# Optimization experiments

Measured on AMD Instinct MI355X. Metric: run time of the kernel, lower is better.

The kernel has to match this reference:

```python
import jax, jax.numpy as jnp
import numpy as np

N = 50000      # nodes
E = 800000     # edges (avg degree 16)
IN = 128       # in_channels
OUT = 2        # out_channels
HID = 100 * OUT  # MAX_CHANNELS * out_channels = 200
MSG_EPS = 1e-7   # GENConv message eps
BN_EPS = 1e-5    # BatchNorm1d eps


def _gen_conv(x, src, dst, w1, b1, g, be, w2, b2):
    """PyG GENConv with defaults: aggr='softmax', t=1.0, msg_norm=False,
    MLP=[c, 2c, c_out] with BatchNorm1d+ReLU between layers (train-mode BN)."""
    # message: relu(x_j) + eps  -> [E, d]
    msg = jnp.maximum(x[src], 0.0) + MSG_EPS
    # scatter softmax over incoming edges of each destination node (t=1)
    m = jax.ops.segment_max(msg, dst, num_segments=N)          # [N, d]
    m = jnp.where(jnp.isfinite(m), m, 0.0)                      # isolated nodes
    ex = jnp.exp(msg - m[dst])                                  # [E, d]
    s = jax.ops.segment_sum(ex, dst, num_segments=N)            # [N, d]
    alpha = ex / (s[dst] + 1e-16)                               # [E, d]
    out = jax.ops.segment_sum(msg * alpha, dst, num_segments=N) # [N, d]
    out = out + x                                               # residual with x_dst
    # MLP: Linear -> BatchNorm(batch stats) -> ReLU -> Linear
    h = out @ w1 + b1                                           # [N, 2d]
    mu = h.mean(axis=0)
    var = h.var(axis=0)
    h = (h - mu) * jax.lax.rsqrt(var + BN_EPS) * g + be
    h = jnp.maximum(h, 0.0)
    return h @ w2 + b2


def setup_inputs() -> dict:
    key = jax.random.key(0)
    ks = jax.random.split(key, 8)
    rn = lambda k, shp, s: jax.random.normal(k, shp, jnp.float32) * s
    mid1, mid2 = 2 * IN, 2 * HID
    return {
        "x": rn(ks[0], (N, IN), 1.0),
        "edge_index": jax.random.randint(ks[1], (2, E), 0, N, jnp.int32),
        "c1_w1": rn(ks[2], (IN, mid1), 0.05), "c1_b1": jnp.zeros((mid1,), jnp.float32),
        "c1_g": jnp.ones((mid1,), jnp.float32), "c1_beta": jnp.zeros((mid1,), jnp.float32),
        "c1_w2": rn(ks[3], (mid1, HID), 0.05), "c1_b2": jnp.zeros((HID,), jnp.float32),
        "c2_w1": rn(ks[4], (HID, mid2), 0.05), "c2_b1": jnp.zeros((mid2,), jnp.float32),
        "c2_g": jnp.ones((mid2,), jnp.float32), "c2_beta": jnp.zeros((mid2,), jnp.float32),
        "c2_w2": rn(ks[5], (mid2, OUT), 0.05), "c2_b2": jnp.zeros((OUT,), jnp.float32),
    }


def reference(x, edge_index, c1_w1, c1_b1, c1_g, c1_beta, c1_w2, c1_b2,
              c2_w1, c2_b1, c2_g, c2_beta, c2_w2, c2_b2):
    src, dst = edge_index[0], edge_index[1]
    h = jnp.maximum(_gen_conv(x, src, dst, c1_w1, c1_b1, c1_g, c1_beta, c1_w2, c1_b2), 0.0)
    # Dropout(p=0.1) is identity in eval mode (deterministic reference)
    return jnp.maximum(_gen_conv(h, src, dst, c2_w1, c2_b1, c2_g, c2_beta, c2_w2, c2_b2), 0.0)
```

## Files before the change

### kernel.cpp

```cpp
#include <hip/hip_runtime.h>
#include <hip/hip_bf16.h>
#include <stdint.h>

#define NNODES 50000
#define NEDGES 800000
#define DIN 128
#define DHID 200
#define MID1 256
#define MID2 400
#define SCAN_NB ((NNODES + 255) / 256)
#define NBB ((NNODES + 127) / 128)
#define RSPLIT 12
#define LOG2E 1.4426950408889634f
#define LN2 0.6931471805599453f
#define GK_SPLIT 96
#define GCH 208
#define GNP 40
#define NBUCK 98
#define BCAP 16384
#define EPB 4096

typedef __hip_bfloat16 bf16;
typedef __attribute__((ext_vector_type(8))) short short8;
typedef __attribute__((ext_vector_type(4))) float floatx4;
typedef unsigned short ushort;

__device__ __forceinline__ float b2f(bf16 v) { return __bfloat162float(v); }
__device__ __forceinline__ bf16 f2b(float v) { return __float2bfloat16(v); }
__device__ __forceinline__ float bits2f(ushort b) {
    unsigned u = ((unsigned)b) << 16;
    return __uint_as_float(u);
}
__device__ __forceinline__ ushort f2bits(float f) {
    bf16 h = __float2bfloat16(f);
    return *(ushort*)&h;
}
__device__ __forceinline__ float ldin(const void* p, size_t i, int f32) {
    return f32 ? ((const float*)p)[i] : __bfloat162float(((const bf16*)p)[i]);
}
__device__ __forceinline__ void ldin4(const void* p, size_t i, int f32, float* v) {
    if (f32) {
        float4 f = *(const float4*)((const float*)p + i);
        v[0] = f.x; v[1] = f.y; v[2] = f.z; v[3] = f.w;
    } else {
        ushort4 u = *(const ushort4*)((const bf16*)p + i);
        v[0] = bits2f(u.x); v[1] = bits2f(u.y); v[2] = bits2f(u.z); v[3] = bits2f(u.w);
    }
}
__device__ __forceinline__ float fexp2(float x) {
#if __has_builtin(__builtin_amdgcn_exp2f)
    return __builtin_amdgcn_exp2f(x);
#else
    return exp2f(x);
#endif
}
__device__ __forceinline__ floatx4 mfma16(short8 a, short8 b, floatx4 c) {
    return __builtin_amdgcn_mfma_f32_16x16x32_bf16(a, b, c, 0, 0, 0);
}
__device__ __forceinline__ void acc4(ushort4 u, float* s, float* p) {
    ushort uu[4];
    *(ushort4*)uu = u;
#pragma unroll
    for (int c = 0; c < 4; c++) {
        float v = bits2f(uu[c]);
        float ee = fexp2(v);
        s[c] += ee;
        p[c] = fmaf(v, ee, p[c]);
    }
}

__global__ __launch_bounds__(256) void bin_kernel(const int* __restrict__ src,
                                                  const int* __restrict__ dst,
                                                  const void* __restrict__ g,
                                                  int* __restrict__ flag,
                                                  unsigned* __restrict__ bbuf,
                                                  int* __restrict__ gcur) {
    __shared__ int cnt[NBUCK], cur[NBUCK];
    int tid = threadIdx.x;
    if (blockIdx.x == 0 && tid == 0)
        *flag = (((const unsigned*)g)[0] == 0x3F800000u) ? 1 : 0;
    if (tid < NBUCK) cnt[tid] = 0;
    __syncthreads();
    int e0 = blockIdx.x * EPB;
    unsigned pk[16];
    int bk[16];
#pragma unroll
    for (int i = 0; i < 16; i++) {
        int e = e0 + i * 256 + tid;
        if (e < NEDGES) {
            int d = dst[e], s = src[e];
            pk[i] = ((unsigned)d << 16) | (unsigned)s;
            bk[i] = d >> 9;
            atomicAdd(&cnt[bk[i]], 1);
        } else {
            bk[i] = -1;
        }
    }
    __syncthreads();
    if (tid < NBUCK) cur[tid] = atomicAdd(&gcur[tid], cnt[tid]);
    __syncthreads();
#pragma unroll
    for (int i = 0; i < 16; i++) {
        if (bk[i] >= 0) {
            int off = atomicAdd(&cur[bk[i]], 1);
            bbuf[(size_t)bk[i] * BCAP + off] = pk[i];
        }
    }
}

__global__ __launch_bounds__(256) void histb_kernel(const unsigned* __restrict__ bbuf,
                                                    const int* __restrict__ gcur,
                                                    int* __restrict__ counts) {
    __shared__ int hc[512];
    int b = blockIdx.x, tid = threadIdx.x;
    int base = b << 9;
    int nn = min(512, NNODES - base);
    for (int i = tid; i < 512; i += 256) hc[i] = 0;
    __syncthreads();
    int cnt = gcur[b];
    const unsigned* eb = bbuf + (size_t)b * BCAP;
    for (int i = tid; i < cnt; i += 256) atomicAdd(&hc[(eb[i] >> 16) - base], 1);
    __syncthreads();
    for (int i = tid; i < nn; i += 256) counts[base + i] = hc[i];
}

__global__ __launch_bounds__(512) void scatterb_kernel(const unsigned* __restrict__ bbuf,
                                                       const int* __restrict__ gcur,
                                                       const int* __restrict__ rowptr,
                                                       int* __restrict__ ssrc) {
    __shared__ int lc[512];
    int b = blockIdx.x, tid = threadIdx.x;
    int base = b << 9;
    int nn = min(512, NNODES - base);
    lc[tid] = (tid < nn) ? rowptr[base + tid] : 0;
    __syncthreads();
    int cnt = gcur[b];
    const unsigned* eb = bbuf + (size_t)b * BCAP;
    for (int i = tid; i < cnt; i += 512) {
        unsigned p = eb[i];
        int node = (int)(p >> 16) - base;
        int idx = atomicAdd(&lc[node], 1);
        ssrc[idx] = (int)(p & 0xFFFFu);
    }
}

__global__ __launch_bounds__(256) void scanA_kernel(const int* __restrict__ counts,
                                                    int* __restrict__ rowptr,
                                                    int* __restrict__ blocksums) {
    __shared__ int sh[256];
    int t = threadIdx.x, b = blockIdx.x;
    int i = b * 256 + t;
    int v = (i < NNODES) ? counts[i] : 0;
    sh[t] = v;
    __syncthreads();
#pragma unroll
    for (int off = 1; off < 256; off <<= 1) {
        int o = (t >= off) ? sh[t - off] : 0;
        __syncthreads();
        sh[t] += o;
        __syncthreads();
    }
    if (i < NNODES) rowptr[i] = sh[t] - v;
    if (t == 255) blocksums[b] = sh[255];
}

__global__ __launch_bounds__(256) void scanC_kernel(int* __restrict__ rowptr,
                                                    const int* __restrict__ blocksums) {
    __shared__ int sh[256];
    int t = threadIdx.x, b = blockIdx.x;
    sh[t] = (t < SCAN_NB) ? blocksums[t] : 0;
    __syncthreads();
#pragma unroll
    for (int off = 1; off < 256; off <<= 1) {
        int o = (t >= off) ? sh[t - off] : 0;
        __syncthreads();
        sh[t] += o;
        __syncthreads();
    }
    int boff = (b > 0) ? sh[b - 1] : 0;
    int i = b * 256 + t;
    if (i < NNODES) rowptr[i] += boff;
    if (i == 0) rowptr[NNODES] = NEDGES;
}

#define TW (DIN * MID1 + MID1 * DHID + DHID * MID2)
__global__ __launch_bounds__(256) void prep_kernel(const void* __restrict__ W1, bf16* __restrict__ Wt1,
                                                   const void* __restrict__ W2, bf16* __restrict__ Wt2,
                                                   const void* __restrict__ W3, bf16* __restrict__ Wt3,
                                                   const void* __restrict__ X, bf16* __restrict__ M1,
                                                   ushort* __restrict__ dummy,
                                                   const int* __restrict__ flag) {
    const int S1 = DIN * MID1, S2 = MID1 * DHID;
    int f32 = *flag;
    int idx = blockIdx.x * 256 + threadIdx.x;
    if (idx < TW) {
        const void* W;
        bf16* Wt;
        int K, N, li;
        if (idx < S1) { W = W1; Wt = Wt1; K = DIN; N = MID1; li = idx; }
        else if (idx < S1 + S2) { W = W2; Wt = Wt2; K = MID1; N = DHID; li = idx - S1; }
        else { W = W3; Wt = Wt3; K = DHID; N = MID2; li = idx - S1 - S2; }
        int k = li / N, n = li - k * N;
        Wt[(size_t)n * K + k] = f2b(ldin(W, li, f32));
    }
    if (idx < DHID) dummy[idx] = 0xC300;
    int i = idx * 4;
    if (i < NNODES * DIN) {
        float v[4];
        ldin4(X, i, f32, v);
        ushort4 o;
        o.x = f2bits((fmaxf(v[0], 0.f) + 1e-7f) * LOG2E);
        o.y = f2bits((fmaxf(v[1], 0.f) + 1e-7f) * LOG2E);
        o.z = f2bits((fmaxf(v[2], 0.f) + 1e-7f) * LOG2E);
        o.w = f2bits((fmaxf(v[3], 0.f) + 1e-7f) * LOG2E);
        *(ushort4*)(M1 + i) = o;
    }
}

__global__ __launch_bounds__(256) void agg1_kernel(const void* __restrict__ X,
                                                   const bf16* __restrict__ M1,
                                                   const int* __restrict__ rowptr,
                                                   const int* __restrict__ ssrc,
                                                   const int* __restrict__ flag,
                                                   bf16* __restrict__ out) {
    int f32 = *flag;
    int hl = threadIdx.x & 31;
    int n = blockIdx.x * 8 + (threadIdx.x >> 5);
    int r0 = rowptr[n];
    int deg = rowptr[n + 1] - r0;
    const char* M1b = (const char*)M1;
    int boff = hl << 3;
    float s[4] = {0.f, 0.f, 0.f, 0.f}, p[4] = {0.f, 0.f, 0.f, 0.f};
    for (int base = 0; base < deg; base += 32) {
        int cnt = min(32, deg - base);
        int eo = ((base + hl < deg) ? ssrc[r0 + base + hl] : 0) << 8;
        int i = 0;
        for (; i + 7 < cnt; i += 8) {
            ushort4 u[8];
#pragma unroll
            for (int k = 0; k < 8; k++) {
                int o = __shfl(eo, i + k, 32) + boff;
                u[k] = *(const ushort4*)(M1b + o);
            }
#pragma unroll
            for (int k = 0; k < 8; k++) acc4(u[k], s, p);
        }
        for (; i < cnt; i++) {
            int o = __shfl(eo, i, 32) + boff;
            acc4(*(const ushort4*)(M1b + o), s, p);
        }
    }
    float xc[4];
    ldin4(X, (size_t)n * DIN + 4 * hl, f32, xc);
    ushort4 o;
    o.x = f2bits(fmaf(LN2, p[0] / (s[0] + 1e-16f), xc[0]));
    o.y = f2bits(fmaf(LN2, p[1] / (s[1] + 1e-16f), xc[1]));
    o.z = f2bits(fmaf(LN2, p[2] / (s[2] + 1e-16f), xc[2]));
    o.w = f2bits(fmaf(LN2, p[3] / (s[3] + 1e-16f), xc[3]));
    *(ushort4*)(out + (size_t)n * DIN + 4 * hl) = o;
}

__global__ __launch_bounds__(256) void agg2_kernel(const bf16* __restrict__ M2,
                                                   const int* __restrict__ rowptr,
                                                   const int* __restrict__ ssrc,
                                                   const ushort* __restrict__ dummy,
                                                   bf16* __restrict__ out) {
    int lane = threadIdx.x & 63;
    int n = blockIdx.x * 4 + (threadIdx.x >> 6);
    int r0 = __builtin_amdgcn_readfirstlane(rowptr[n]);
    int deg = __builtin_amdgcn_readfirstlane(rowptr[n + 1]) - r0;
    bool act = lane < 50;
    int boff = (act ? lane : 49) << 3;
    const char* M2b = (const char*)M2;
    const char* dp = (const char*)dummy;
    float s[4] = {0.f, 0.f, 0.f, 0.f}, p[4] = {0.f, 0.f, 0.f, 0.f};
    int nfull = deg >> 3;
    for (int b = 0; b < nfull; b++) {
        const int* ep = ssrc + r0 + (b << 3);
        ushort4 u[8];
#pragma unroll
        for (int k = 0; k < 8; k++)
            u[k] = *(const ushort4*)(M2b + (size_t)((unsigned)ep[k] * 400u) + boff);
#pragma unroll
        for (int k = 0; k < 8; k++) acc4(u[k], s, p);
    }
    int rem = deg & 7;
    if (rem) {
        const int* ep = ssrc + r0 + (nfull << 3);
        ushort4 u[8];
#pragma unroll
        for (int k = 0; k < 8; k++) {
            const char* rp = (k < rem) ? (M2b + (size_t)((unsigned)ep[k] * 400u)) : dp;
            u[k] = *(const ushort4*)(rp + boff);
        }
#pragma unroll
        for (int k = 0; k < 8; k++) acc4(u[k], s, p);
    }
    if (act) {
        ushort4 u = *(const ushort4*)(M2b + (size_t)n * 400 + boff);
        float vn[4] = {bits2f(u.x), bits2f(u.y), bits2f(u.z), bits2f(u.w)};
        ushort4 o;
        o.x = f2bits(LN2 * (p[0] / (s[0] + 1e-16f) + vn[0]) - 1e-7f);
        o.y = f2bits(LN2 * (p[1] / (s[1] + 1e-16f) + vn[1]) - 1e-7f);
        o.z = f2bits(LN2 * (p[2] / (s[2] + 1e-16f) + vn[2]) - 1e-7f);
        o.w = f2bits(LN2 * (p[3] / (s[3] + 1e-16f) + vn[3]) - 1e-7f);
        *(ushort4*)(out + (size_t)n * DHID + 4 * lane) = o;
    }
}

template <int MODE, int NT, int KK, int NCOL>
__global__ __launch_bounds__(512, 4) void bgemm(const bf16* __restrict__ A,
                                                const bf16* __restrict__ Bt,
                                                const void* __restrict__ bias,
                                                const int* __restrict__ flag,
                                                const float* __restrict__ sc,
                                                const float* __restrict__ offs,
                                                const void* __restrict__ w2,
                                                bf16* __restrict__ Out, int ostride,
                                                float* __restrict__ psum,
                                                float* __restrict__ psq,
                                                float* __restrict__ fscr, int M) {
    constexpr int KP = (KK + 31) & ~31;
    constexpr int KS = KP / 32;
    constexpr int KV8 = KP / 8;
    __shared__ short Bs[NT * 16][KP + 8];
    int f32 = *flag;
    int tid = threadIdx.x;
    int cb = blockIdx.y * NCOL;

    for (int idx = tid; idx < NT * 16 * KV8; idx += 512) {
        int col = idx / KV8, kq = (idx - col * KV8) * 8;
        uint4 v = {0, 0, 0, 0};
        if (col < NCOL && kq < KK) v = *(const uint4*)(Bt + (size_t)(cb + col) * KK + kq);
        *(uint4*)&Bs[col][kq] = v;
    }
    __syncthreads();

    int w = tid >> 6, L = tid & 63;
    int lm = L & 15, q = L >> 4;
    int rw = blockIdx.x * 128 + w * 16;
    int ar = rw + lm;
    bool rok = ar < M;

    uint4 af[KS];
#pragma unroll
    for (int s = 0; s < KS; s++) {
        int k = s * 32 + q * 8;
        af[s] = (uint4){0, 0, 0, 0};
        if (rok && k + 8 <= KK) af[s] = *(const uint4*)(A + (size_t)ar * KK + k);
    }

    floatx4 acc[NT];
#pragma unroll
    for (int t = 0; t < NT; t++) acc[t] = (floatx4){0.f, 0.f, 0.f, 0.f};

#pragma unroll
    for (int s = 0; s < KS; s++) {
        short8 as;
        if (MODE == 1) {
            int ch = s * 32 + q * 8;
            float4 sA = *(const float4*)(sc + ch), sB = *(const float4*)(sc + ch + 4);
            float4 oA = *(const float4*)(offs + ch), oB = *(const float4*)(offs + ch + 4);
            float scv[8] = {sA.x, sA.y, sA.z, sA.w, sB.x, sB.y, sB.z, sB.w};
            float ofv[8] = {oA.x, oA.y, oA.z, oA.w, oB.x, oB.y, oB.z, oB.w};
            ushort us[8];
            *(uint4*)us = af[s];
#pragma unroll
            for (int j = 0; j < 8; j++)
                us[j] = f2bits(fmaxf(fmaf(bits2f(us[j]), scv[j], ofv[j]), 0.f));
            as = *(short8*)us;
        } else {
            as = *(short8*)&af[s];
        }
#pragma unroll
        for (int t = 0; t < NT; t++) {
            short8 bf = *(const short8*)&Bs[t * 16 + lm][s * 32 + q * 8];
            acc[t] = mfma16(as, bf, acc[t]);
        }
    }

    if (MODE == 0) {
#pragma unroll
        for (int t = 0; t < NT; t++) {
            int col = t * 16 + lm;
            float bb = ldin(bias, col, f32);
            float cs = 0.f, cq = 0.f;
#pragma unroll
            for (int r = 0; r < 4; r++) {
                int gm = rw + q * 4 + r;
                if (gm < M) {
                    float v = acc[t][r] + bb;
                    Out[(size_t)gm * ostride + col] = f2b(v);
                    cs += v;
                    cq += v * v;
                }
            }
            cs += __shfl_xor(cs, 16, 64); cq += __shfl_xor(cq, 16, 64);
            cs += __shfl_xor(cs, 32, 64); cq += __shfl_xor(cq, 32, 64);
            if (q == 0) {
                psum[(size_t)(blockIdx.x * 8 + w) * (NT * 16) + col] = cs;
                psq[(size_t)(blockIdx.x * 8 + w) * (NT * 16) + col] = cq;
            }
        }
    }
    if (MODE == 1) {
#pragma unroll
        for (int t = 0; t < NT; t++) {
            int col = t * 16 + lm;
            if (col < NCOL) {
                int gg = cb + col;
                float bb = ldin(bias, gg, f32);
#pragma unroll
                for (int r = 0; r < 4; r++) {
                    int gm = rw + q * 4 + r;
                    if (gm < M) {
                        float v = acc[t][r] + bb;
                        Out[(size_t)gm * ostride + gg] = f2b((fmaxf(v, 0.f) + 1e-7f) * LOG2E);
                    }
                }
            }
        }
    }
    if (MODE == 2) {
        float s0[4] = {0.f, 0.f, 0.f, 0.f}, s1[4] = {0.f, 0.f, 0.f, 0.f};
#pragma unroll
        for (int t = 0; t < NT; t++) {
            int col = t * 16 + lm;
            if (col < NCOL) {
                int gg = cb + col;
                float bb = ldin(bias, gg, f32);
                float scv = sc[gg], ofv = offs[gg];
                float w20 = ldin(w2, 2 * gg, f32), w21 = ldin(w2, 2 * gg + 1, f32);
#pragma unroll
                for (int r = 0; r < 4; r++) {
                    float vn = fmaxf((acc[t][r] + bb) * scv + ofv, 0.f);
                    s0[r] = fmaf(vn, w20, s0[r]);
                    s1[r] = fmaf(vn, w21, s1[r]);
                }
            }
        }
#pragma unroll
        for (int d = 1; d < 16; d <<= 1) {
#pragma unroll
            for (int r = 0; r < 4; r++) {
                s0[r] += __shfl_xor(s0[r], d, 64);
                s1[r] += __shfl_xor(s1[r], d, 64);
            }
        }
        if (lm == 0) {
#pragma unroll
            for (int r = 0; r < 4; r++) {
                int gm = rw + q * 4 + r;
                if (gm < M) {
                    fscr[(size_t)gm * 8 + blockIdx.y * 2 + 0] = s0[r];
                    fscr[(size_t)gm * 8 + blockIdx.y * 2 + 1] = s1[r];
                }
            }
        }
    }
}

__global__ __launch_bounds__(256) void stats_reduce(const float* __restrict__ psum,
                                                    const float* __restrict__ psq,
                                                    float* __restrict__ bnsum,
                                                    float* __restrict__ bnsumsq,
                                                    int NB, int NC) {
    __shared__ float shs[4][64], shq[4][64];
    int cc = threadIdx.x & 63;
    int c = blockIdx.x * 64 + cc;
    int ro = threadIdx.x >> 6;
    int chunk = (NB + RSPLIT - 1) / RSPLIT;
    int b0 = blockIdx.y * chunk;
    int b1 = min(b0 + chunk, NB);
    float s = 0.f, sq = 0.f;
    if (c < NC) {
        for (int b = b0 + ro; b < b1; b += 4) {
            s += psum[(size_t)b * NC + c];
            sq += psq[(size_t)b * NC + c];
        }
    }
    shs[ro][cc] = s;
    shq[ro][cc] = sq;
    __syncthreads();
    if (threadIdx.x < 64) {
        int gc = blockIdx.x * 64 + threadIdx.x;
        if (gc < NC) {
            int t = threadIdx.x;
            float ts = shs[0][t] + shs[1][t] + shs[2][t] + shs[3][t];
            float tq = shq[0][t] + shq[1][t] + shq[2][t] + shq[3][t];
            atomicAdd(&bnsum[gc], ts);
            atomicAdd(&bnsumsq[gc], tq);
        }
    }
}

__global__ void bn_finish(const float* __restrict__ sum, const float* __restrict__ sumsq,
                          const void* __restrict__ g, const void* __restrict__ be,
                          const int* __restrict__ flag,
                          float* __restrict__ sc, float* __restrict__ off, int C) {
    int f32 = *flag;
    int c = blockIdx.x * blockDim.x + threadIdx.x;
    if (c < C) {
        float mu = sum[c] / (float)NNODES;
        float var = fmaxf(sumsq[c] / (float)NNODES - mu * mu, 0.f);
        float rstd = rsqrtf(var + 1e-5f);
        float s = rstd * ldin(g, c, f32);
        sc[c] = s;
        off[c] = ldin(be, c, f32) - mu * s;
    }
}

__global__ __launch_bounds__(512) void gram_kernel(const bf16* __restrict__ X,
                                                   float* __restrict__ pg) {
    __shared__ short T[GCH][GNP];
    int tid = threadIdx.x;
    int w = tid >> 6, L = tid & 63;
    int lm = L & 15, q = L >> 4;
    floatx4 acc[2][13];
#pragma unroll
    for (int c = 0; c < 2; c++)
#pragma unroll
        for (int t = 0; t < 13; t++) acc[c][t] = (floatx4){0.f, 0.f, 0.f, 0.f};

    const int chunks = (NNODES + 32 * GK_SPLIT - 1) / (32 * GK_SPLIT);
    int base0 = blockIdx.x * chunks * 32;
    for (int ch = 0; ch < chunks; ch++) {
        int nb = base0 + ch * 32;
#pragma unroll
        for (int p = 0; p < 4; p++) {
            int idx = tid + p * 512;
            if (idx < 1600) {
                int nl = idx & 31, cq = idx >> 5;
                int gn = nb + nl;
                ushort4 u = {0, 0, 0, 0};
                if (gn < NNODES) u = *(const ushort4*)(X + (size_t)gn * DHID + cq * 4);
                T[cq * 4 + 0][nl] = (short)u.x;
                T[cq * 4 + 1][nl] = (short)u.y;
                T[cq * 4 + 2][nl] = (short)u.z;
                T[cq * 4 + 3][nl] = (short)u.w;
            }
        }
        if (tid < 256) {
            int nl = tid & 31, c = 200 + (tid >> 5);
            int gn = nb + nl;
            T[c][nl] = (c == 200 && gn < NNODES) ? (short)0x3F80 : (short)0;
        }
        __syncthreads();
        short8 af[13];
#pragma unroll
        for (int t = 0; t < 13; t++) af[t] = *(const short8*)&T[t * 16 + lm][q * 8];
#pragma unroll
        for (int c = 0; c < 2; c++) {
            int cj = w + c * 8;
            if (cj < 13) {
                short8 bf = *(const short8*)&T[cj * 16 + lm][q * 8];
#pragma unroll
                for (int t = 0; t < 13; t++) acc[c][t] = mfma16(af[t], bf, acc[c][t]);
            }
        }
        __syncthreads();
    }
    float* pgb = pg + (size_t)blockIdx.x * (GCH * GCH);
#pragma unroll
    for (int c = 0; c < 2; c++) {
        int cj = w + c * 8;
        if (cj < 13) {
#pragma unroll
            for (int t = 0; t < 13; t++)
#pragma unroll
                for (int r = 0; r < 4; r++)
                    pgb[(size_t)(t * 16 + q * 4 + r) * GCH + cj * 16 + lm] = acc[c][t][r];
        }
    }
}

__global__ void greduce_kernel(const float* __restrict__ pg, float* __restrict__ G) {
    int e = blockIdx.x * 256 + threadIdx.x;
    if (e < GCH * GCH) {
        float s = 0.f;
        for (int b = 0; b < GK_SPLIT; b++) s += pg[(size_t)b * (GCH * GCH) + e];
        G[e] = s;
    }
}

__global__ __launch_bounds__(256) void bn2_finish(const float* __restrict__ G,
                                                  const bf16* __restrict__ Wt3,
                                                  const void* __restrict__ b1,
                                                  const void* __restrict__ g,
                                                  const void* __restrict__ be,
                                                  const int* __restrict__ flag,
                                                  float* __restrict__ sc,
                                                  float* __restrict__ off) {
    __shared__ float wl[200];
    __shared__ float red[256];
    __shared__ float dsh;
    int f32 = *flag;
    int c = blockIdx.x;
    int t = threadIdx.x;
    if (t < 200) wl[t] = b2f(Wt3[(size_t)c * DHID + t]);
    __syncthreads();
    float di = 0.f;
    if (t <= 200) {
        const float* Gr = G + (size_t)t * GCH;
        for (int j = 0; j < 200; j++) di = fmaf(Gr[j], wl[j], di);
    }
    red[t] = (t < 200) ? wl[t] * di : 0.f;
    if (t == 200) dsh = di;
    __syncthreads();
    for (int o = 128; o > 0; o >>= 1) {
        if (t < o) red[t] += red[t + o];
        __syncthreads();
    }
    if (t == 0) {
        float d = dsh;
        float bc = ldin(b1, c, f32);
        float mu = d / (float)NNODES + bc;
        float eh2 = (red[0] + 2.f * bc * d) / (float)NNODES + bc * bc;
        float var = fmaxf(eh2 - mu * mu, 0.f);
        float rstd = rsqrtf(var + 1e-5f);
        float s = rstd * ldin(g, c, f32);
        sc[c] = s;
        off[c] = ldin(be, c, f32) - mu * s;
    }
}

__global__ void final_combine(const float* __restrict__ fscr, const void* __restrict__ b2,
                              const int* __restrict__ flag, void* __restrict__ outp, int M) {
    int f32 = *flag;
    int n = blockIdx.x * 256 + threadIdx.x;
    if (n < M) {
        const float* f = fscr + (size_t)n * 8;
        float v0 = fmaxf(f[0] + f[2] + f[4] + f[6] + ldin(b2, 0, f32), 0.f);
        float v1 = fmaxf(f[1] + f[3] + f[5] + f[7] + ldin(b2, 1, f32), 0.f);
        if (f32) {
            ((float*)outp)[2 * n] = v0;
            ((float*)outp)[2 * n + 1] = v1;
        } else {
            ((bf16*)outp)[2 * n] = f2b(v0);
            ((bf16*)outp)[2 * n + 1] = f2b(v1);
        }
    }
}

extern "C" void kernel_launch(void* const* d_in, const int* in_sizes, int n_in,
                              void* d_out, int out_size, void* d_ws, size_t ws_size,
                              hipStream_t stream) {
    const void* x = d_in[0];
    const int* ei = (const int*)d_in[1];
    const void* c1_w1 = d_in[2];
    const void* c1_b1 = d_in[3];
    const void* c1_g = d_in[4];
    const void* c1_be = d_in[5];
    const void* c1_w2 = d_in[6];
    const void* c1_b2 = d_in[7];
    const void* c2_w1 = d_in[8];
    const void* c2_b1 = d_in[9];
    const void* c2_g = d_in[10];
    const void* c2_be = d_in[11];
    const void* c2_w2 = d_in[12];
    const void* c2_b2 = d_in[13];

    const int* src = ei;
    const int* dst = ei + NEDGES;

    uint8_t* w = (uint8_t*)d_ws;
    int* rowptr = (int*)(w + 0);
    int* counts = (int*)(w + 204800);
    bf16* wT1 = (bf16*)(w + 204800);
    bf16* wT2 = (bf16*)(w + 270336);
    bf16* wT3 = (bf16*)(w + 409600);
    int* ssrc = (int*)(w + 614400);
    float* bnbuf = (float*)(w + 3814400);
    float* sum1 = bnbuf, *sumsq1 = bnbuf + 256;
    int* gcur = (int*)(bnbuf + 512);
    float* sc1 = bnbuf + 1312, *off1 = bnbuf + 1568;
    float* sc2 = bnbuf + 1824, *off2 = bnbuf + 2224;
    int* flag_in = (int*)(bnbuf + 2624);
    int* blocksums = (int*)(bnbuf + 2640);
    ushort* dummyrow = (ushort*)(bnbuf + 2840);
    uint8_t* bufA = w + 3830784;
    uint8_t* bufB = w + 23830784;
    unsigned* bbuf = (unsigned*)bufA;
    bf16* out1 = (bf16*)bufA;
    bf16* h1 = (bf16*)bufA;
    float* fscr = (float*)bufA;
    float* pg = (float*)bufA;
    float* Gm = (float*)(bufA + 17000000);
    bf16* M1 = (bf16*)bufB;
    bf16* t1 = (bf16*)bufB;
    bf16* out2 = (bf16*)bufB;
    float* ps1 = (float*)(bufA + 12800000);
    float* pq1 = ps1 + (size_t)NBB * 8 * MID1;

    hipMemsetAsync(bnbuf, 0, 1312 * sizeof(float), stream);

    bin_kernel<<<(NEDGES + EPB - 1) / EPB, 256, 0, stream>>>(src, dst, c1_g, flag_in,
                                                             bbuf, gcur);
    histb_kernel<<<NBUCK, 256, 0, stream>>>(bbuf, gcur, counts);
    scanA_kernel<<<SCAN_NB, 256, 0, stream>>>(counts, rowptr, blocksums);
    scanC_kernel<<<SCAN_NB, 256, 0, stream>>>(rowptr, blocksums);
    scatterb_kernel<<<NBUCK, 512, 0, stream>>>(bbuf, gcur, rowptr, ssrc);

    prep_kernel<<<(NNODES * DIN / 4 + 255) / 256, 256, 0, stream>>>(
        c1_w1, wT1, c1_w2, wT2, c2_w1, wT3, x, M1, dummyrow, flag_in);

    agg1_kernel<<<NNODES / 8, 256, 0, stream>>>(x, M1, rowptr, ssrc, flag_in, out1);
    bgemm<0, 16, 128, 256><<<dim3(NBB, 1), 512, 0, stream>>>(
        out1, wT1, c1_b1, flag_in, nullptr, nullptr, nullptr,
        t1, MID1, ps1, pq1, nullptr, NNODES);
    stats_reduce<<<dim3((MID1 + 63) / 64, RSPLIT), 256, 0, stream>>>(ps1, pq1, sum1, sumsq1,
                                                                     NBB * 8, MID1);
    bn_finish<<<1, 256, 0, stream>>>(sum1, sumsq1, c1_g, c1_be, flag_in, sc1, off1, MID1);
    bgemm<1, 7, 256, 100><<<dim3(NBB, 2), 512, 0, stream>>>(
        t1, wT2, c1_b2, flag_in, sc1, off1, nullptr,
        h1, DHID, nullptr, nullptr, nullptr, NNODES);

    agg2_kernel<<<NNODES / 4, 256, 0, stream>>>(h1, rowptr, ssrc, dummyrow, out2);
    gram_kernel<<<GK_SPLIT, 512, 0, stream>>>(out2, pg);
    greduce_kernel<<<(GCH * GCH + 255) / 256, 256, 0, stream>>>(pg, Gm);
    bn2_finish<<<MID2, 256, 0, stream>>>(Gm, wT3, c2_b1, c2_g, c2_be, flag_in, sc2, off2);
    bgemm<2, 7, 200, 100><<<dim3(NBB, 4), 512, 0, stream>>>(
        out2, wT3, c2_b1, flag_in, sc2, off2, c2_w2,
        nullptr, 0, nullptr, nullptr, fscr, NNODES);
    final_combine<<<(NNODES + 255) / 256, 256, 0, stream>>>(fscr, c2_b2, flag_in,
                                                            d_out, NNODES);
}
```

Measured before the change: 374.4 us.

## Store gather sources in column-sliced layout to shrink per-edge gather footprint

The message tensors for both aggregation stages are now written in column-sliced layouts: 4 slices of 32 channels for layer 1 and 5 slices of 40 channels for layer 2, with each node's slice stored contiguously. The aggregation kernels become 64-thread blocks in which several nodes each gather only one slice, two edges per iteration. Block ordering is arranged so the slices are processed in groups, meant to keep the gathered working set small enough to stay resident in cache. The cost is more launched blocks, repeated loads of rowptr and ssrc for each slice, lanes left idle on nodes of uneven degree, and the loss of the deeper 8-way load unrolling.

```diff
diff --git a/kernel.cpp b/kernel.cpp
--- a/kernel.cpp
+++ b/kernel.cpp
@@ -213,98 +213,91 @@
         o.y = f2bits((fmaxf(v[1], 0.f) + 1e-7f) * LOG2E);
         o.z = f2bits((fmaxf(v[2], 0.f) + 1e-7f) * LOG2E);
         o.w = f2bits((fmaxf(v[3], 0.f) + 1e-7f) * LOG2E);
-        *(ushort4*)(M1 + i) = o;
-    }
-}
-
-__global__ __launch_bounds__(256) void agg1_kernel(const void* __restrict__ X,
-                                                   const bf16* __restrict__ M1,
-                                                   const int* __restrict__ rowptr,
-                                                   const int* __restrict__ ssrc,
-                                                   const int* __restrict__ flag,
-                                                   bf16* __restrict__ out) {
+        int node = i >> 7, c = i & 127;
+        int s = c >> 5, c2 = c & 31;
+        *(ushort4*)(M1 + (size_t)s * 1600000 + (size_t)node * 32 + c2) = o;
+    }
+}
+
+__global__ __launch_bounds__(64) void agg1_kernel(const void* __restrict__ X,
+                                                  const bf16* __restrict__ M1,
+                                                  const int* __restrict__ rowptr,
+                                                  const int* __restrict__ ssrc,
+                                                  const ushort* __restrict__ dummy,
+                                                  const int* __restrict__ flag,
+                                                  bf16* __restrict__ out) {
     int f32 = *flag;
-    int hl = threadIdx.x & 31;
-    int n = blockIdx.x * 8 + (threadIdx.x >> 5);
+    int lane = threadIdx.x;
+    int g = lane >> 3, k = lane & 7;
+    int bx = blockIdx.x;
+    int xs = bx & 7;
+    int s = xs >> 1;
+    int ng = (bx >> 3) * 2 + (xs & 1);
+    int n = ng * 8 + g;
     int r0 = rowptr[n];
     int deg = rowptr[n + 1] - r0;
-    const char* M1b = (const char*)M1;
-    int boff = hl << 3;
-    float s[4] = {0.f, 0.f, 0.f, 0.f}, p[4] = {0.f, 0.f, 0.f, 0.f};
-    for (int base = 0; base < deg; base += 32) {
-        int cnt = min(32, deg - base);
-        int eo = ((base + hl < deg) ? ssrc[r0 + base + hl] : 0) << 8;
-        int i = 0;
-        for (; i + 7 < cnt; i += 8) {
-            ushort4 u[8];
-#pragma unroll
-            for (int k = 0; k < 8; k++) {
-                int o = __shfl(eo, i + k, 32) + boff;
-                u[k] = *(const ushort4*)(M1b + o);
-            }
-#pragma unroll
-            for (int k = 0; k < 8; k++) acc4(u[k], s, p);
-        }
-        for (; i < cnt; i++) {
-            int o = __shfl(eo, i, 32) + boff;
-            acc4(*(const ushort4*)(M1b + o), s, p);
-        }
-    }
+    const char* base = (const char*)M1 + (size_t)s * 3200000;
+    const char* dm = (const char*)dummy + k * 8;
+    float sa[4] = {0.f, 0.f, 0.f, 0.f}, pa[4] = {0.f, 0.f, 0.f, 0.f};
+    for (int i = 0;; i += 2) {
+        bool a0 = i < deg, a1 = i + 1 < deg;
+        if (!__any(a0)) break;
+        int e0 = ssrc[a0 ? r0 + i : 0];
+        int e1 = ssrc[a1 ? r0 + i + 1 : 0];
+        const char* p0 = a0 ? base + (size_t)(unsigned)e0 * 64u + k * 8 : dm;
+        const char* p1 = a1 ? base + (size_t)(unsigned)e1 * 64u + k * 8 : dm;
+        ushort4 u0 = *(const ushort4*)p0;
+        ushort4 u1 = *(const ushort4*)p1;
+        acc4(u0, sa, pa);
+        acc4(u1, sa, pa);
+    }
+    int c0 = s * 32 + k * 4;
     float xc[4];
-    ldin4(X, (size_t)n * DIN + 4 * hl, f32, xc);
+    ldin4(X, (size_t)n * DIN + c0, f32, xc);
     ushort4 o;
-    o.x = f2bits(fmaf(LN2, p[0] / (s[0] + 1e-16f), xc[0]));
-    o.y = f2bits(fmaf(LN2, p[1] / (s[1] + 1e-16f), xc[1]));
-    o.z = f2bits(fmaf(LN2, p[2] / (s[2] + 1e-16f), xc[2]));
-    o.w = f2bits(fmaf(LN2, p[3] / (s[3] + 1e-16f), xc[3]));
-    *(ushort4*)(out + (size_t)n * DIN + 4 * hl) = o;
-}
-
-__global__ __launch_bounds__(256) void agg2_kernel(const bf16* __restrict__ M2,
-                                                   const int* __restrict__ rowptr,
-                                                   const int* __restrict__ ssrc,
-                                                   const ushort* __restrict__ dummy,
-                                                   bf16* __restrict__ out) {
-    int lane = threadIdx.x & 63;
-    int n = blockIdx.x * 4 + (threadIdx.x >> 6);
-    int r0 = __builtin_amdgcn_readfirstlane(rowptr[n]);
-    int deg = __builtin_amdgcn_readfirstlane(rowptr[n + 1]) - r0;
+    o.x = f2bits(fmaf(LN2, pa[0] / (sa[0] + 1e-16f), xc[0]));
+    o.y = f2bits(fmaf(LN2, pa[1] / (sa[1] + 1e-16f), xc[1]));
+    o.z = f2bits(fmaf(LN2, pa[2] / (sa[2] + 1e-16f), xc[2]));
+    o.w = f2bits(fmaf(LN2, pa[3] / (sa[3] + 1e-16f), xc[3]));
+    *(ushort4*)(out + (size_t)n * DIN + c0) = o;
+}
+
+__global__ __launch_bounds__(64) void agg2_kernel(const bf16* __restrict__ M2,
+                                                  const int* __restrict__ rowptr,
+                                                  const int* __restrict__ ssrc,
+                                                  const ushort* __restrict__ dummy,
+                                                  bf16* __restrict__ out) {
+    int lane = threadIdx.x;
+    int g = lane / 10, k = lane - g * 10;
     bool act = lane < 50;
-    int boff = (act ? lane : 49) << 3;
-    const char* M2b = (const char*)M2;
-    const char* dp = (const char*)dummy;
-    float s[4] = {0.f, 0.f, 0.f, 0.f}, p[4] = {0.f, 0.f, 0.f, 0.f};
-    int nfull = deg >> 3;
-    for (int b = 0; b < nfull; b++) {
-        const int* ep = ssrc + r0 + (b << 3);
-        ushort4 u[8];
-#pragma unroll
-        for (int k = 0; k < 8; k++)
-            u[k] = *(const ushort4*)(M2b + (size_t)((unsigned)ep[k] * 400u) + boff);
-#pragma unroll
-        for (int k = 0; k < 8; k++) acc4(u[k], s, p);
-    }
-    int rem = deg & 7;
-    if (rem) {
-        const int* ep = ssrc + r0 + (nfull << 3);
-        ushort4 u[8];
-#pragma unroll
-        for (int k = 0; k < 8; k++) {
-            const char* rp = (k < rem) ? (M2b + (size_t)((unsigned)ep[k] * 400u)) : dp;
-            u[k] = *(const ushort4*)(rp + boff);
-        }
-#pragma unroll
-        for (int k = 0; k < 8; k++) acc4(u[k], s, p);
+    int s = blockIdx.y;
+    int n = blockIdx.x * 5 + (act ? g : 0);
+    int r0 = rowptr[n];
+    int deg = act ? (rowptr[n + 1] - r0) : 0;
+    const char* base = (const char*)M2 + (size_t)s * 4000000;
+    const char* dm = (const char*)dummy + k * 8;
+    float sa[4] = {0.f, 0.f, 0.f, 0.f}, pa[4] = {0.f, 0.f, 0.f, 0.f};
+    for (int i = 0;; i += 2) {
+        bool a0 = i < deg, a1 = i + 1 < deg;
+        if (!__any(a0)) break;
+        int e0 = ssrc[a0 ? r0 + i : 0];
+        int e1 = ssrc[a1 ? r0 + i + 1 : 0];
+        const char* p0 = a0 ? base + (size_t)(unsigned)e0 * 80u + k * 8 : dm;
+        const char* p1 = a1 ? base + (size_t)(unsigned)e1 * 80u + k * 8 : dm;
+        ushort4 u0 = *(const ushort4*)p0;
+        ushort4 u1 = *(const ushort4*)p1;
+        acc4(u0, sa, pa);
+        acc4(u1, sa, pa);
     }
     if (act) {
-        ushort4 u = *(const ushort4*)(M2b + (size_t)n * 400 + boff);
+        ushort4 u = *(const ushort4*)(base + (size_t)n * 80 + k * 8);
         float vn[4] = {bits2f(u.x), bits2f(u.y), bits2f(u.z), bits2f(u.w)};
         ushort4 o;
-        o.x = f2bits(LN2 * (p[0] / (s[0] + 1e-16f) + vn[0]) - 1e-7f);
-        o.y = f2bits(LN2 * (p[1] / (s[1] + 1e-16f) + vn[1]) - 1e-7f);
-        o.z = f2bits(LN2 * (p[2] / (s[2] + 1e-16f) + vn[2]) - 1e-7f);
-        o.w = f2bits(LN2 * (p[3] / (s[3] + 1e-16f) + vn[3]) - 1e-7f);
-        *(ushort4*)(out + (size_t)n * DHID + 4 * lane) = o;
+        o.x = f2bits(LN2 * (pa[0] / (sa[0] + 1e-16f) + vn[0]) - 1e-7f);
+        o.y = f2bits(LN2 * (pa[1] / (sa[1] + 1e-16f) + vn[1]) - 1e-7f);
+        o.z = f2bits(LN2 * (pa[2] / (sa[2] + 1e-16f) + vn[2]) - 1e-7f);
+        o.w = f2bits(LN2 * (pa[3] / (sa[3] + 1e-16f) + vn[3]) - 1e-7f);
+        *(ushort4*)(out + (size_t)n * DHID + s * 40 + k * 4) = o;
     }
 }
 
@@ -410,12 +403,14 @@
             if (col < NCOL) {
                 int gg = cb + col;
                 float bb = ldin(bias, gg, f32);
+                int slc = gg / 40, cc = gg - slc * 40;
+                bf16* op = Out + (size_t)slc * 2000000 + cc;
 #pragma unroll
                 for (int r = 0; r < 4; r++) {
                     int gm = rw + q * 4 + r;
                     if (gm < M) {
                         float v = acc[t][r] + bb;
-                        Out[(size_t)gm * ostride + gg] = f2b((fmaxf(v, 0.f) + 1e-7f) * LOG2E);
+                        op[(size_t)gm * 40] = f2b((fmaxf(v, 0.f) + 1e-7f) * LOG2E);
                     }
                 }
             }
@@ -704,7 +699,7 @@
     prep_kernel<<<(NNODES * DIN / 4 + 255) / 256, 256, 0, stream>>>(
         c1_w1, wT1, c1_w2, wT2, c2_w1, wT3, x, M1, dummyrow, flag_in);
 
-    agg1_kernel<<<NNODES / 8, 256, 0, stream>>>(x, M1, rowptr, ssrc, flag_in, out1);
+    agg1_kernel<<<25000, 64, 0, stream>>>(x, M1, rowptr, ssrc, dummyrow, flag_in, out1);
     bgemm<0, 16, 128, 256><<<dim3(NBB, 1), 512, 0, stream>>>(
         out1, wT1, c1_b1, flag_in, nullptr, nullptr, nullptr,
         t1, MID1, ps1, pq1, nullptr, NNODES);
@@ -715,7 +710,7 @@
         t1, wT2, c1_b2, flag_in, sc1, off1, nullptr,
         h1, DHID, nullptr, nullptr, nullptr, NNODES);
 
-    agg2_kernel<<<NNODES / 4, 256, 0, stream>>>(h1, rowptr, ssrc, dummyrow, out2);
+    agg2_kernel<<<dim3(10000, 5), 64, 0, stream>>>(h1, rowptr, ssrc, dummyrow, out2);
     gram_kernel<<<GK_SPLIT, 512, 0, stream>>>(out2, pg);
     greduce_kernel<<<(GCH * GCH + 255) / 256, 256, 0, stream>>>(pg, Gm);
     bn2_finish<<<MID2, 256, 0, stream>>>(Gm, wT3, c2_b1, c2_g, c2_be, flag_in, sc2, off2);
```

Result: slower. 402.4 us (+7.5%).

## Split layer-1 message features into 32-channel slabs and restructure aggregation

Applied to the files above, without the earlier changes.

The prep kernel now writes the relu'd message tensor as four channel slabs of 32 features each ([4][N][32]), so each slab is a compact 64-byte-per-node array. agg1 is rewritten so a wavefront handles one node and one slab, with 8 lanes per edge covering 32 channels and 8 edge groups processed in parallel, followed by a cross-group shuffle reduction. Blocks are interleaved so consecutive blocks touch the same slab, shrinking the working set per phase to improve L2 hit rate on random gathers. The trade is that the edge lists are read four times and a reduction step is added. Invalid edges read a dummy row whose value is large and negative.

```diff
diff --git a/kernel.cpp b/kernel.cpp
--- a/kernel.cpp
+++ b/kernel.cpp
@@ -213,7 +213,9 @@
         o.y = f2bits((fmaxf(v[1], 0.f) + 1e-7f) * LOG2E);
         o.z = f2bits((fmaxf(v[2], 0.f) + 1e-7f) * LOG2E);
         o.w = f2bits((fmaxf(v[3], 0.f) + 1e-7f) * LOG2E);
-        *(ushort4*)(M1 + i) = o;
+        int node = i >> 7, c = i & 127;
+        int s = c >> 5, c2 = c & 31;
+        *(ushort4*)(M1 + (size_t)s * 1600000 + (size_t)node * 32 + c2) = o;
     }
 }
 
@@ -221,43 +223,54 @@
                                                    const bf16* __restrict__ M1,
                                                    const int* __restrict__ rowptr,
                                                    const int* __restrict__ ssrc,
+                                                   const ushort* __restrict__ dummy,
                                                    const int* __restrict__ flag,
                                                    bf16* __restrict__ out) {
     int f32 = *flag;
-    int hl = threadIdx.x & 31;
-    int n = blockIdx.x * 8 + (threadIdx.x >> 5);
-    int r0 = rowptr[n];
-    int deg = rowptr[n + 1] - r0;
-    const char* M1b = (const char*)M1;
-    int boff = hl << 3;
-    float s[4] = {0.f, 0.f, 0.f, 0.f}, p[4] = {0.f, 0.f, 0.f, 0.f};
-    for (int base = 0; base < deg; base += 32) {
-        int cnt = min(32, deg - base);
-        int eo = ((base + hl < deg) ? ssrc[r0 + base + hl] : 0) << 8;
-        int i = 0;
-        for (; i + 7 < cnt; i += 8) {
-            ushort4 u[8];
-#pragma unroll
-            for (int k = 0; k < 8; k++) {
-                int o = __shfl(eo, i + k, 32) + boff;
-                u[k] = *(const ushort4*)(M1b + o);
-            }
-#pragma unroll
-            for (int k = 0; k < 8; k++) acc4(u[k], s, p);
-        }
-        for (; i < cnt; i++) {
-            int o = __shfl(eo, i, 32) + boff;
-            acc4(*(const ushort4*)(M1b + o), s, p);
-        }
-    }
-    float xc[4];
-    ldin4(X, (size_t)n * DIN + 4 * hl, f32, xc);
-    ushort4 o;
-    o.x = f2bits(fmaf(LN2, p[0] / (s[0] + 1e-16f), xc[0]));
-    o.y = f2bits(fmaf(LN2, p[1] / (s[1] + 1e-16f), xc[1]));
-    o.z = f2bits(fmaf(LN2, p[2] / (s[2] + 1e-16f), xc[2]));
-    o.w = f2bits(fmaf(LN2, p[3] / (s[3] + 1e-16f), xc[3]));
-    *(ushort4*)(out + (size_t)n * DIN + 4 * hl) = o;
+    int tid = threadIdx.x;
+    int w = tid >> 6, lane = tid & 63;
+    int g = lane >> 3, k = lane & 7;
+    int bx = blockIdx.x;
+    int xs = bx & 7;
+    int s = xs >> 1;
+    int ni = (bx >> 3) * 2 + (xs & 1);
+    int n = ni * 4 + w;
+    int r0 = __builtin_amdgcn_readfirstlane(rowptr[n]);
+    int deg = __builtin_amdgcn_readfirstlane(rowptr[n + 1]) - r0;
+    const char* base = (const char*)M1 + (size_t)s * 3200000;
+    const char* dm = (const char*)dummy + k * 8;
+    float sa[4] = {0.f, 0.f, 0.f, 0.f}, pa[4] = {0.f, 0.f, 0.f, 0.f};
+    for (int i = 0; i < deg; i += 16) {
+        int e0 = i + g, e1 = i + 8 + g;
+        bool v0 = e0 < deg, v1 = e1 < deg;
+        int i0 = ssrc[r0 + (v0 ? e0 : 0)];
+        int i1 = ssrc[r0 + (v1 ? e1 : 0)];
+        const char* p0 = v0 ? base + (size_t)(unsigned)i0 * 64u + k * 8 : dm;
+        const char* p1 = v1 ? base + (size_t)(unsigned)i1 * 64u + k * 8 : dm;
+        ushort4 u0 = *(const ushort4*)p0;
+        ushort4 u1 = *(const ushort4*)p1;
+        acc4(u0, sa, pa);
+        acc4(u1, sa, pa);
+    }
+#pragma unroll
+    for (int d = 8; d < 64; d <<= 1) {
+#pragma unroll
+        for (int c = 0; c < 4; c++) {
+            sa[c] += __shfl_xor(sa[c], d, 64);
+            pa[c] += __shfl_xor(pa[c], d, 64);
+        }
+    }
+    if (g == 0) {
+        int c0 = s * 32 + k * 4;
+        float xc[4];
+        ldin4(X, (size_t)n * DIN + c0, f32, xc);
+        ushort4 o;
+        o.x = f2bits(fmaf(LN2, pa[0] / (sa[0] + 1e-16f), xc[0]));
+        o.y = f2bits(fmaf(LN2, pa[1] / (sa[1] + 1e-16f), xc[1]));
+        o.z = f2bits(fmaf(LN2, pa[2] / (sa[2] + 1e-16f), xc[2]));
+        o.w = f2bits(fmaf(LN2, pa[3] / (sa[3] + 1e-16f), xc[3]));
+        *(ushort4*)(out + (size_t)n * DIN + c0) = o;
+    }
 }
 
 __global__ __launch_bounds__(256) void agg2_kernel(const bf16* __restrict__ M2,
@@ -704,7 +717,7 @@
     prep_kernel<<<(NNODES * DIN / 4 + 255) / 256, 256, 0, stream>>>(
         c1_w1, wT1, c1_w2, wT2, c2_w1, wT3, x, M1, dummyrow, flag_in);
 
-    agg1_kernel<<<NNODES / 8, 256, 0, stream>>>(x, M1, rowptr, ssrc, flag_in, out1);
+    agg1_kernel<<<50000, 256, 0, stream>>>(x, M1, rowptr, ssrc, dummyrow, flag_in, out1);
     bgemm<0, 16, 128, 256><<<dim3(NBB, 1), 512, 0, stream>>>(
         out1, wT1, c1_b1, flag_in, nullptr, nullptr, nullptr,
         t1, MID1, ps1, pq1, nullptr, NNODES);
```

New measurement: 412.8 us. +10.3%, slower.
